# Kernel tuning notes

Hardware: AMD Instinct MI355X
Metric: run time of the kernel (lower is better)

Reference implementation:

```python
import jax, jax.numpy as jnp
import numpy as np
from itertools import product

N_VOX = 100000
GRID = 128
KS = 3
K = KS ** 3
INC_MAX, OUTC_MAX = 64, 96
RUNTIME_INC, RUNTIME_OUTC = 48, 64


def _build_rulebook(rng):
    flat = rng.choice(GRID ** 3, size=N_VOX, replace=False).astype(np.int64)
    coords = np.stack(np.unravel_index(flat, (GRID, GRID, GRID)), axis=1)  # [N,3]
    # Dense lookup table: flat coord -> voxel index (or -1).
    table = np.full(GRID ** 3, -1, dtype=np.int32)
    table[flat] = np.arange(N_VOX, dtype=np.int32)
    offsets = np.array(list(product([-1, 0, 1], repeat=3)), dtype=np.int64)  # [27,3]
    idx = np.empty((K, N_VOX), dtype=np.int32)
    for k, off in enumerate(offsets):
        nb = coords + off  # stride=1, dilation=1
        valid = np.all((nb >= 0) & (nb < GRID), axis=1)
        nb_flat = (nb[:, 0] * GRID + nb[:, 1]) * GRID + nb[:, 2]
        nb_flat = np.where(valid, nb_flat, 0)
        idx[k] = np.where(valid, table[nb_flat], -1)
    return idx


def setup_inputs() -> dict:
    key = jax.random.key(0)
    kf, kw = jax.random.split(key)
    features = jax.random.normal(kf, (N_VOX, RUNTIME_INC), dtype=jnp.float32)
    # Full kernel param [K, inc_max, outc_max]; runtime-sliced inside reference.
    std = 1.0 / np.sqrt(INC_MAX * K)
    kernel = jax.random.uniform(kw, (K, INC_MAX, OUTC_MAX), dtype=jnp.float32,
                                minval=-std, maxval=std)
    idx = jnp.asarray(_build_rulebook(np.random.default_rng(0)))  # [K, N]
    return {"features": features, "kernel": kernel, "idx": idx,
            "runtime_inc": RUNTIME_INC, "runtime_outc": RUNTIME_OUTC}


def reference(features, kernel, idx, runtime_inc, runtime_outc):
    # Dynamic channel slicing (static Python ints -> jit friendly).
    w = kernel[:, :runtime_inc, :runtime_outc]          # [K, Ci, Co]
    mask = idx >= 0                                      # [K, N]
    safe = jnp.where(mask, idx, 0)
    # Gather -> per-offset GEMM -> accumulate (scatter is identity: out idx == n).
    gathered = features[safe] * mask[..., None].astype(features.dtype)  # [K, N, Ci]
    out = jnp.einsum('knc,kco->no', gathered, w)         # [N, Co]
    return out
```

## Files before the change

kernel.cpp:

```cpp
#include <hip/hip_runtime.h>
#include <hip/hip_bf16.h>

#define NVOX       100000
#define INC        48
#define INC_MAX    64
#define OUTC       64
#define OUTC_MAX   96
#define KOFF       27
#define WTB_K      3072
#define WTB_ELEMS  (KOFF * WTB_K)
#define ZROW_FLOATS 48
#define WS_NEED    ((size_t)WTB_ELEMS * 2 + ZROW_FLOATS * 4)
#define WTB_PREP_BLKS  (WTB_ELEMS / 256)
#define MAIN_BLOCKS 782

typedef __attribute__((ext_vector_type(8)))  short short8;
typedef __attribute__((ext_vector_type(4)))  float floatx4;
typedef __attribute__((ext_vector_type(16))) float floatx16;

__device__ __forceinline__ short f2bf(float f) {
    union { __hip_bfloat16 h; short s; } u;
    u.h = __float2bfloat16(f);
    return u.s;
}

__global__ void __launch_bounds__(256)
prep_w(const float* __restrict__ wk, short* __restrict__ wtb,
       float* __restrict__ zrowf)
{
    int b = blockIdx.x;
    if (b < WTB_PREP_BLKS) {
        int t = b * 256 + threadIdx.x;
        int k = t / WTB_K, r = t % WTB_K;
        int chunk = r >> 3, j = r & 7;
        int f = chunk >> 6, lane = chunk & 63;
        int ks = f >> 1, nt = f & 1;
        int c = ks * 16 + (lane >> 5) * 8 + j;
        int o = nt * 32 + (lane & 31);
        wtb[t] = f2bf(wk[k * (INC_MAX * OUTC_MAX) + c * OUTC_MAX + o]);
    } else if (threadIdx.x < ZROW_FLOATS) {
        zrowf[threadIdx.x] = 0.f;
    }
}

__global__ void __launch_bounds__(256, 3)
spconv_main(const float* __restrict__ feat, const short* __restrict__ wtb,
            const float* __restrict__ zrowf, const int* __restrict__ idx,
            float* __restrict__ out)
{
    __shared__ short Bs[4][WTB_K];

    const int tid  = threadIdx.x;
    const int lane = tid & 63;
    const int wave = tid >> 6;
    const int l32  = lane & 31;
    const int hi   = lane >> 5;

    int bid = blockIdx.x;
    int sb  = (bid < 776) ? ((bid & 7) * 97 + (bid >> 3)) : bid;

    const int m0   = (sb * 4 + wave) * 32;
    const bool act = (m0 < NVOX);
    const int rr   = act ? (m0 + l32) : 0;

    floatx16 acc[2];
    #pragma unroll
    for (int nt = 0; nt < 2; ++nt)
        #pragma unroll
        for (int r = 0; r < 16; ++r) acc[nt][r] = 0.f;

    floatx4 F[2][3][2];
    short8  bst[2][2];
    int     rowg[4];
    bool    va4[4];
    bool    ca[2];

    auto ldrow = [&](int k) {
        int t0 = idx[k * NVOX + rr];
        rowg[k & 3] = t0;
        va4[k & 3] = __any(t0 >= 0);
    };
    auto aload = [&](int k) {
        bool v = va4[k & 3];
        ca[k & 1] = v;
        if (v) {
            int t = rowg[k & 3];
            const float* p = (t >= 0) ? (feat + (size_t)t * INC) : zrowf;
            #pragma unroll
            for (int ks = 0; ks < 3; ++ks) {
                const floatx4* q = (const floatx4*)(p + ks * 16 + hi * 8);
                F[k & 1][ks][0] = q[0];
                F[k & 1][ks][1] = q[1];
            }
        }
    };
    auto bload = [&](int k) {
        bst[k & 1][0] = *(const short8*)(wtb + k * WTB_K + tid * 8);
        if (tid < 128)
            bst[k & 1][1] = *(const short8*)(wtb + k * WTB_K + 2048 + tid * 8);
    };
    auto compute = [&](int k) {
        if (!ca[k & 1]) return;
        #pragma unroll
        for (int ks = 0; ks < 3; ++ks) {
            short8 b0 = *(const short8*)&Bs[k & 3][(ks * 128 + lane) * 8];
            short8 b1 = *(const short8*)&Bs[k & 3][(ks * 128 + 64 + lane) * 8];
            short8 a;
            #pragma unroll
            for (int j = 0; j < 4; ++j) {
                a[j]     = f2bf(F[k & 1][ks][0][j]);
                a[4 + j] = f2bf(F[k & 1][ks][1][j]);
            }
            acc[0] = __builtin_amdgcn_mfma_f32_32x32x16_bf16(a, b0, acc[0], 0, 0, 0);
            acc[1] = __builtin_amdgcn_mfma_f32_32x32x16_bf16(a, b1, acc[1], 0, 0, 0);
        }
    };

    ldrow(0); ldrow(1); ldrow(2); ldrow(3);
    bload(0); bload(1);
    aload(0); aload(1);

    #pragma unroll
    for (int j = 0; j < 14; ++j) {
        const int kk = 2 * j;

        *(short8*)&Bs[kk & 3][tid * 8] = bst[0][0];
        if (tid < 128) *(short8*)&Bs[kk & 3][2048 + tid * 8] = bst[0][1];
        if (kk + 1 < KOFF) {
            *(short8*)&Bs[(kk + 1) & 3][tid * 8] = bst[1][0];
            if (tid < 128) *(short8*)&Bs[(kk + 1) & 3][2048 + tid * 8] = bst[1][1];
        }
        __syncthreads();

        if (kk + 2 < KOFF) bload(kk + 2);
        if (kk + 3 < KOFF) bload(kk + 3);
        if (kk + 4 < KOFF) ldrow(kk + 4);
        if (kk + 5 < KOFF) ldrow(kk + 5);

        compute(kk);
        if (kk + 2 < KOFF) aload(kk + 2);
        if (kk + 1 < KOFF) {
            compute(kk + 1);
            if (kk + 3 < KOFF) aload(kk + 3);
        }
    }

    if (act) {
        #pragma unroll
        for (int nt = 0; nt < 2; ++nt) {
            #pragma unroll
            for (int r = 0; r < 16; ++r) {
                int row = (r & 3) + 8 * (r >> 2) + 4 * hi;
                out[(m0 + row) * OUTC + nt * 32 + l32] = acc[nt][r];
            }
        }
    }
}

__global__ void __launch_bounds__(256)
spconv_fallback(const float* __restrict__ feat, const float* __restrict__ wk,
                const int* __restrict__ idx, float* __restrict__ out)
{
    int t = blockIdx.x * 256 + threadIdx.x;
    if (t >= NVOX * OUTC) return;
    int n = t >> 6, o = t & 63;
    float s = 0.f;
    for (int k = 0; k < KOFF; ++k) {
        int g = idx[k * NVOX + n];
        if (g >= 0) {
            const float* fr = feat + g * INC;
            const float* wr = wk + k * (INC_MAX * OUTC_MAX) + o;
            #pragma unroll 8
            for (int c = 0; c < INC; ++c) s += fr[c] * wr[c * OUTC_MAX];
        }
    }
    out[t] = s;
}

extern "C" void kernel_launch(void* const* d_in, const int* in_sizes, int n_in,
                              void* d_out, int out_size, void* d_ws, size_t ws_size,
                              hipStream_t stream) {
    const float* feat = (const float*)d_in[0];
    const float* wk   = (const float*)d_in[1];
    const int*   idx  = (const int*)d_in[2];
    float* out = (float*)d_out;

    if (ws_size >= WS_NEED) {
        short* wtb   = (short*)d_ws;
        float* zrowf = (float*)((char*)d_ws + (size_t)WTB_ELEMS * 2);
        prep_w<<<WTB_PREP_BLKS + 1, 256, 0, stream>>>(wk, wtb, zrowf);
        spconv_main<<<MAIN_BLOCKS, 256, 0, stream>>>(feat, wtb, zrowf, idx, out);
    } else {
        spconv_fallback<<<(NVOX * OUTC + 255) / 256, 256, 0, stream>>>(feat, wk, idx, out);
    }
}
```

Measured before the change: 110.4 us.

## Process 64 rows per wave with two M-tiles sharing B fragments

Each wave now computes two 32-row tiles, so every LDS weight fragment feeds four MFMAs instead of two. Blocks shrink to 128 threads (2 waves) while keeping the same block count, and the weight staging loop is reshaped to three 1024-element chunks. This halves LDS weight reads and staging work per output row. The cost is roughly double the accumulator and feature register footprint, which may reduce occupancy and the latency hiding for the irregular gathers.

```diff
diff --git a/kernel.cpp b/kernel.cpp
--- a/kernel.cpp
+++ b/kernel.cpp
@@ -43,7 +43,7 @@
     }
 }
 
-__global__ void __launch_bounds__(256, 3)
+__global__ void __launch_bounds__(128, 2)
 spconv_main(const float* __restrict__ feat, const short* __restrict__ wtb,
             const float* __restrict__ zrowf, const int* __restrict__ idx,
             float* __restrict__ out)
@@ -59,45 +59,54 @@
     int bid = blockIdx.x;
     int sb  = (bid < 776) ? ((bid & 7) * 97 + (bid >> 3)) : bid;
 
-    const int m0   = (sb * 4 + wave) * 32;
-    const bool act = (m0 < NVOX);
-    const int rr   = act ? (m0 + l32) : 0;
-
-    floatx16 acc[2];
+    const int m0   = (sb * 2 + wave) * 64;
+    const bool act  = (m0 < NVOX);
+    const bool act1 = (m0 + 32 < NVOX);
+    const int rr0  = act  ? (m0 + l32)      : 0;
+    const int rr1  = act1 ? (m0 + 32 + l32) : 0;
+
+    floatx16 acc[2][2];
     #pragma unroll
-    for (int nt = 0; nt < 2; ++nt)
-        #pragma unroll
-        for (int r = 0; r < 16; ++r) acc[nt][r] = 0.f;
-
-    floatx4 F[2][3][2];
-    short8  bst[2][2];
-    int     rowg[4];
+    for (int g = 0; g < 2; ++g)
+        #pragma unroll
+        for (int nt = 0; nt < 2; ++nt)
+            #pragma unroll
+            for (int r = 0; r < 16; ++r) acc[g][nt][r] = 0.f;
+
+    floatx4 F[2][2][3][2];
+    short8  bst[2][3];
+    int     rowg[4][2];
     bool    va4[4];
     bool    ca[2];
 
     auto ldrow = [&](int k) {
-        int t0 = idx[k * NVOX + rr];
-        rowg[k & 3] = t0;
-        va4[k & 3] = __any(t0 >= 0);
+        int t0 = idx[k * NVOX + rr0];
+        int t1 = act1 ? idx[k * NVOX + rr1] : -1;
+        rowg[k & 3][0] = t0;
+        rowg[k & 3][1] = t1;
+        va4[k & 3] = __any((t0 >= 0) || (t1 >= 0));
     };
     auto aload = [&](int k) {
         bool v = va4[k & 3];
         ca[k & 1] = v;
         if (v) {
-            int t = rowg[k & 3];
-            const float* p = (t >= 0) ? (feat + (size_t)t * INC) : zrowf;
-            #pragma unroll
-            for (int ks = 0; ks < 3; ++ks) {
-                const floatx4* q = (const floatx4*)(p + ks * 16 + hi * 8);
-                F[k & 1][ks][0] = q[0];
-                F[k & 1][ks][1] = q[1];
+            #pragma unroll
+            for (int g = 0; g < 2; ++g) {
+                int t = rowg[k & 3][g];
+                const float* p = (t >= 0) ? (feat + (size_t)t * INC) : zrowf;
+                #pragma unroll
+                for (int ks = 0; ks < 3; ++ks) {
+                    const floatx4* q = (const floatx4*)(p + ks * 16 + hi * 8);
+                    F[k & 1][g][ks][0] = q[0];
+                    F[k & 1][g][ks][1] = q[1];
+                }
             }
         }
     };
     auto bload = [&](int k) {
-        bst[k & 1][0] = *(const short8*)(wtb + k * WTB_K + tid * 8);
-        if (tid < 128)
-            bst[k & 1][1] = *(const short8*)(wtb + k * WTB_K + 2048 + tid * 8);
+        #pragma unroll
+        for (int p = 0; p < 3; ++p)
+            bst[k & 1][p] = *(const short8*)(wtb + k * WTB_K + p * 1024 + tid * 8);
     };
     auto compute = [&](int k) {
         if (!ca[k & 1]) return;
@@ -105,14 +114,18 @@
         for (int ks = 0; ks < 3; ++ks) {
             short8 b0 = *(const short8*)&Bs[k & 3][(ks * 128 + lane) * 8];
             short8 b1 = *(const short8*)&Bs[k & 3][(ks * 128 + 64 + lane) * 8];
-            short8 a;
+            short8 a0, a1;
             #pragma unroll
             for (int j = 0; j < 4; ++j) {
-                a[j]     = f2bf(F[k & 1][ks][0][j]);
-                a[4 + j] = f2bf(F[k & 1][ks][1][j]);
-            }
-            acc[0] = __builtin_amdgcn_mfma_f32_32x32x16_bf16(a, b0, acc[0], 0, 0, 0);
-            acc[1] = __builtin_amdgcn_mfma_f32_32x32x16_bf16(a, b1, acc[1], 0, 0, 0);
+                a0[j]     = f2bf(F[k & 1][0][ks][0][j]);
+                a0[4 + j] = f2bf(F[k & 1][0][ks][1][j]);
+                a1[j]     = f2bf(F[k & 1][1][ks][0][j]);
+                a1[4 + j] = f2bf(F[k & 1][1][ks][1][j]);
+            }
+            acc[0][0] = __builtin_amdgcn_mfma_f32_32x32x16_bf16(a0, b0, acc[0][0], 0, 0, 0);
+            acc[0][1] = __builtin_amdgcn_mfma_f32_32x32x16_bf16(a0, b1, acc[0][1], 0, 0, 0);
+            acc[1][0] = __builtin_amdgcn_mfma_f32_32x32x16_bf16(a1, b0, acc[1][0], 0, 0, 0);
+            acc[1][1] = __builtin_amdgcn_mfma_f32_32x32x16_bf16(a1, b1, acc[1][1], 0, 0, 0);
         }
     };
 
@@ -124,11 +137,13 @@
     for (int j = 0; j < 14; ++j) {
         const int kk = 2 * j;
 
-        *(short8*)&Bs[kk & 3][tid * 8] = bst[0][0];
-        if (tid < 128) *(short8*)&Bs[kk & 3][2048 + tid * 8] = bst[0][1];
+        #pragma unroll
+        for (int p = 0; p < 3; ++p)
+            *(short8*)&Bs[kk & 3][p * 1024 + tid * 8] = bst[0][p];
         if (kk + 1 < KOFF) {
-            *(short8*)&Bs[(kk + 1) & 3][tid * 8] = bst[1][0];
-            if (tid < 128) *(short8*)&Bs[(kk + 1) & 3][2048 + tid * 8] = bst[1][1];
+            #pragma unroll
+            for (int p = 0; p < 3; ++p)
+                *(short8*)&Bs[(kk + 1) & 3][p * 1024 + tid * 8] = bst[1][p];
         }
         __syncthreads();
 
@@ -151,7 +166,17 @@
             #pragma unroll
             for (int r = 0; r < 16; ++r) {
                 int row = (r & 3) + 8 * (r >> 2) + 4 * hi;
-                out[(m0 + row) * OUTC + nt * 32 + l32] = acc[nt][r];
+                out[(m0 + row) * OUTC + nt * 32 + l32] = acc[0][nt][r];
+            }
+        }
+    }
+    if (act1) {
+        #pragma unroll
+        for (int nt = 0; nt < 2; ++nt) {
+            #pragma unroll
+            for (int r = 0; r < 16; ++r) {
+                int row = (r & 3) + 8 * (r >> 2) + 4 * hi;
+                out[(m0 + 32 + row) * OUTC + nt * 32 + l32] = acc[1][nt][r];
             }
         }
     }
@@ -189,7 +214,7 @@
         short* wtb   = (short*)d_ws;
         float* zrowf = (float*)((char*)d_ws + (size_t)WTB_ELEMS * 2);
         prep_w<<<WTB_PREP_BLKS + 1, 256, 0, stream>>>(wk, wtb, zrowf);
-        spconv_main<<<MAIN_BLOCKS, 256, 0, stream>>>(feat, wtb, zrowf, idx, out);
+        spconv_main<<<MAIN_BLOCKS, 128, 0, stream>>>(feat, wtb, zrowf, idx, out);
     } else {
         spconv_fallback<<<(NVOX * OUTC + 255) / 256, 256, 0, stream>>>(feat, wk, idx, out);
     }
```

After: 118.9 us. 1.08x slower.
